# Performance work log

Measured on AMD Instinct MI355X. Metric: run time of the kernel, lower is better.

The kernel has to match this reference:

```python
import jax, jax.numpy as jnp
import numpy as np


def setup_inputs() -> dict:
    key = jax.random.key(0)
    k1, k2 = jax.random.split(key)
    N = 2_000_000
    rotation = jax.random.normal(k1, (N, 3, 3), dtype=jnp.float32)
    # learned parameter: eye(3) + 0.001 * randn(3,3)
    mat = jnp.eye(3, dtype=jnp.float32) + 0.001 * jax.random.normal(k2, (3, 3), dtype=jnp.float32)
    return {"rotation": rotation, "mat": mat}


def reference(rotation, mat):
    # new_mat[n] = rotation[n] @ mat   (mat broadcast over the batch)
    new_mat = jnp.einsum('nab,bc->nac', rotation, mat)
    # batched 3x3 SVD; polar orthogonal factor U @ V^T
    U, S, Vh = jnp.linalg.svd(new_mat, full_matrices=False)
    out = jnp.einsum('nab,nbc->nac', U, Vh)  # Vh is already V^T
    logdet = jnp.zeros((rotation.shape[0],), dtype=rotation.dtype)
    return out, logdet
```

## Files before the change

### kernel.cpp

```cpp
#include <hip/hip_runtime.h>
#include <math.h>

constexpr int BLOCK = 256;

__global__ __launch_bounds__(BLOCK) void polar3x3_kernel(
    const float* __restrict__ rot,
    const float* __restrict__ mat,
    float* __restrict__ outq,
    float* __restrict__ logdet,
    int N)
{
    __shared__ float lds[BLOCK * 9];
    const int tid = threadIdx.x;
    const long long base = (long long)blockIdx.x * BLOCK;
    const int rem = (int)(N - base);
    const int nmat = rem < BLOCK ? rem : BLOCK;
    const int nflt = nmat * 9;
    const int nv4 = nflt >> 2;

    const float* gsrc = rot + base * 9;
    {
        const float4* g4 = (const float4*)gsrc;
        float4* l4 = (float4*)lds;
        for (int i = tid; i < nv4; i += BLOCK) l4[i] = g4[i];
        for (int i = (nv4 << 2) + tid; i < nflt; i += BLOCK) lds[i] = gsrc[i];
    }

    const float m0=mat[0], m1=mat[1], m2=mat[2], m3=mat[3], m4=mat[4],
                m5=mat[5], m6=mat[6], m7=mat[7], m8=mat[8];
    const double dM = (double)m0*((double)m4*m8-(double)m5*m7)
                    - (double)m1*((double)m3*m8-(double)m5*m6)
                    + (double)m2*((double)m3*m7-(double)m4*m6);
    __syncthreads();

    const bool active = tid < nmat;
    float x0=1.f,x1=0.f,x2=0.f,x3=0.f,x4=1.f,x5=0.f,x6=0.f,x7=0.f,x8=1.f;
    float detA = 1.f;

    if (active) {
        const float* r = &lds[tid * 9];
        const float r0=r[0],r1=r[1],r2=r[2],r3=r[3],r4=r[4],r5=r[5],r6=r[6],r7=r[7],r8=r[8];
        const double dR = (double)r0*((double)r4*r8-(double)r5*r7)
                        - (double)r1*((double)r3*r8-(double)r5*r6)
                        + (double)r2*((double)r3*r7-(double)r4*r6);
        detA = (float)(dR * dM);
        x0=fmaf(r0,m0,fmaf(r1,m3,r2*m6));
        x1=fmaf(r0,m1,fmaf(r1,m4,r2*m7));
        x2=fmaf(r0,m2,fmaf(r1,m5,r2*m8));
        x3=fmaf(r3,m0,fmaf(r4,m3,r5*m6));
        x4=fmaf(r3,m1,fmaf(r4,m4,r5*m7));
        x5=fmaf(r3,m2,fmaf(r4,m5,r5*m8));
        x6=fmaf(r6,m0,fmaf(r7,m3,r8*m6));
        x7=fmaf(r6,m1,fmaf(r7,m4,r8*m7));
        x8=fmaf(r6,m2,fmaf(r7,m5,r8*m8));
    }

    #pragma unroll
    for (int it = 0; it < 5; ++it) {
        const float c0=fmaf(x4,x8,-x5*x7), c1=fmaf(x5,x6,-x3*x8), c2=fmaf(x3,x7,-x4*x6);
        const float c3=fmaf(x2,x7,-x1*x8), c4=fmaf(x0,x8,-x2*x6), c5=fmaf(x1,x6,-x0*x7);
        const float c6=fmaf(x1,x5,-x2*x4), c7=fmaf(x2,x3,-x0*x5), c8=fmaf(x0,x4,-x1*x3);
        const float det = (it==0) ? detA : fmaf(x0,c0,fmaf(x1,c1,x2*c2));
        const float adet = fmaxf(fabsf(det), 1e-30f);
        float nX2, nC2;
        { const float a=fmaf(x1,x1,x0*x0), b=fmaf(x3,x3,x2*x2),
                      e=fmaf(x5,x5,x4*x4), d=fmaf(x7,x7,x6*x6);
          nX2=(a+b)+(e+fmaf(x8,x8,d)); }
        { const float a=fmaf(c1,c1,c0*c0), b=fmaf(c3,c3,c2*c2),
                      e=fmaf(c5,c5,c4*c4), d=fmaf(c7,c7,c6*c6);
          nC2=(a+b)+(e+fmaf(c8,c8,d)); }
        const float h  = __builtin_amdgcn_rsqf(adet);
        const float pr = __builtin_amdgcn_sqrtf(__builtin_amdgcn_sqrtf(
                             nC2*__builtin_amdgcn_rcpf(nX2)));
        const float qr = __builtin_amdgcn_sqrtf(__builtin_amdgcn_sqrtf(
                             nX2*__builtin_amdgcn_rcpf(nC2)));
        const float s = 0.5f*pr*h;
        const float t = copysignf(0.5f*qr*h, det);
        x0=fmaf(s,x0,t*c0); x1=fmaf(s,x1,t*c1); x2=fmaf(s,x2,t*c2);
        x3=fmaf(s,x3,t*c3); x4=fmaf(s,x4,t*c4); x5=fmaf(s,x5,t*c5);
        x6=fmaf(s,x6,t*c6); x7=fmaf(s,x7,t*c7); x8=fmaf(s,x8,t*c8);
    }
    {
        const float c0=fmaf(x4,x8,-x5*x7), c1=fmaf(x5,x6,-x3*x8), c2=fmaf(x3,x7,-x4*x6);
        const float c3=fmaf(x2,x7,-x1*x8), c4=fmaf(x0,x8,-x2*x6), c5=fmaf(x1,x6,-x0*x7);
        const float c6=fmaf(x1,x5,-x2*x4), c7=fmaf(x2,x3,-x0*x5), c8=fmaf(x0,x4,-x1*x3);
        const float det = fmaf(x0,c0,fmaf(x1,c1,x2*c2));
        const float t = 0.5f*__builtin_amdgcn_rcpf(det);
        x0=fmaf(0.5f,x0,t*c0); x1=fmaf(0.5f,x1,t*c1); x2=fmaf(0.5f,x2,t*c2);
        x3=fmaf(0.5f,x3,t*c3); x4=fmaf(0.5f,x4,t*c4); x5=fmaf(0.5f,x5,t*c5);
        x6=fmaf(0.5f,x6,t*c6); x7=fmaf(0.5f,x7,t*c7); x8=fmaf(0.5f,x8,t*c8);
    }

    if (active) {
        float* w = &lds[tid * 9];
        w[0]=x0; w[1]=x1; w[2]=x2; w[3]=x3; w[4]=x4;
        w[5]=x5; w[6]=x6; w[7]=x7; w[8]=x8;
    }
    __syncthreads();

    float* gdst = outq + base * 9;
    {
        float4* g4 = (float4*)gdst;
        const float4* l4 = (const float4*)lds;
        for (int i = tid; i < nv4; i += BLOCK) g4[i] = l4[i];
        for (int i = (nv4 << 2) + tid; i < nflt; i += BLOCK) gdst[i] = lds[i];
    }

    if (base + tid < N) logdet[base + tid] = 0.0f;
}

extern "C" void kernel_launch(void* const* d_in, const int* in_sizes, int n_in,
                              void* d_out, int out_size, void* d_ws, size_t ws_size,
                              hipStream_t stream) {
    const float* rot = (const float*)d_in[0];
    const float* mat = (const float*)d_in[1];
    float* out = (float*)d_out;
    const int N = in_sizes[0] / 9;
    float* logdet = out + (long long)N * 9;
    const int nblocks = (N + BLOCK - 1) / BLOCK;
    polar3x3_kernel<<<nblocks, BLOCK, 0, stream>>>(rot, mat, out, logdet, N);
}
```

Measured before the change: 138.1 us.

## Use per-wave direct global-to-LDS loads and drop block barriers

Each wave now stages its own 64 matrices through a private LDS slice, loading them with global_load_lds (direct DMA into LDS, no VGPR round trip) and waiting with s_waitcnt instead of __syncthreads. Block-wide barriers are gone, so waves proceed independently. A separate path handles the partial tail wave with direct per-thread global loads and stores. The cost is reliance on exact LDS layout and manual waitcnt correctness, plus an added code path for the tail.

```diff
diff --git a/kernel.cpp b/kernel.cpp
--- a/kernel.cpp
+++ b/kernel.cpp
@@ -3,57 +3,35 @@
 
 constexpr int BLOCK = 256;
 
-__global__ __launch_bounds__(BLOCK) void polar3x3_kernel(
-    const float* __restrict__ rot,
-    const float* __restrict__ mat,
-    float* __restrict__ outq,
-    float* __restrict__ logdet,
-    int N)
+typedef __attribute__((address_space(3))) uint32_t lds_u32_t;
+typedef __attribute__((address_space(1))) const uint32_t glb_u32_t;
+
+__device__ __forceinline__ void polar_core(
+    const float r0, const float r1, const float r2,
+    const float r3, const float r4, const float r5,
+    const float r6, const float r7, const float r8,
+    const float m0, const float m1, const float m2,
+    const float m3, const float m4, const float m5,
+    const float m6, const float m7, const float m8,
+    const double dM,
+    float& x0, float& x1, float& x2,
+    float& x3, float& x4, float& x5,
+    float& x6, float& x7, float& x8)
 {
-    __shared__ float lds[BLOCK * 9];
-    const int tid = threadIdx.x;
-    const long long base = (long long)blockIdx.x * BLOCK;
-    const int rem = (int)(N - base);
-    const int nmat = rem < BLOCK ? rem : BLOCK;
-    const int nflt = nmat * 9;
-    const int nv4 = nflt >> 2;
+    const double dR = (double)r0*((double)r4*r8-(double)r5*r7)
+                    - (double)r1*((double)r3*r8-(double)r5*r6)
+                    + (double)r2*((double)r3*r7-(double)r4*r6);
+    const float detA = (float)(dR * dM);
 
-    const float* gsrc = rot + base * 9;
-    {
-        const float4* g4 = (const float4*)gsrc;
-        float4* l4 = (float4*)lds;
-        for (int i = tid; i < nv4; i += BLOCK) l4[i] = g4[i];
-        for (int i = (nv4 << 2) + tid; i < nflt; i += BLOCK) lds[i] = gsrc[i];
-    }
-
-    const float m0=mat[0], m1=mat[1], m2=mat[2], m3=mat[3], m4=mat[4],
-                m5=mat[5], m6=mat[6], m7=mat[7], m8=mat[8];
-    const double dM = (double)m0*((double)m4*m8-(double)m5*m7)
-                    - (double)m1*((double)m3*m8-(double)m5*m6)
-                    + (double)m2*((double)m3*m7-(double)m4*m6);
-    __syncthreads();
-
-    const bool active = tid < nmat;
-    float x0=1.f,x1=0.f,x2=0.f,x3=0.f,x4=1.f,x5=0.f,x6=0.f,x7=0.f,x8=1.f;
-    float detA = 1.f;
-
-    if (active) {
-        const float* r = &lds[tid * 9];
-        const float r0=r[0],r1=r[1],r2=r[2],r3=r[3],r4=r[4],r5=r[5],r6=r[6],r7=r[7],r8=r[8];
-        const double dR = (double)r0*((double)r4*r8-(double)r5*r7)
-                        - (double)r1*((double)r3*r8-(double)r5*r6)
-                        + (double)r2*((double)r3*r7-(double)r4*r6);
-        detA = (float)(dR * dM);
-        x0=fmaf(r0,m0,fmaf(r1,m3,r2*m6));
-        x1=fmaf(r0,m1,fmaf(r1,m4,r2*m7));
-        x2=fmaf(r0,m2,fmaf(r1,m5,r2*m8));
-        x3=fmaf(r3,m0,fmaf(r4,m3,r5*m6));
-        x4=fmaf(r3,m1,fmaf(r4,m4,r5*m7));
-        x5=fmaf(r3,m2,fmaf(r4,m5,r5*m8));
-        x6=fmaf(r6,m0,fmaf(r7,m3,r8*m6));
-        x7=fmaf(r6,m1,fmaf(r7,m4,r8*m7));
-        x8=fmaf(r6,m2,fmaf(r7,m5,r8*m8));
-    }
+    x0=fmaf(r0,m0,fmaf(r1,m3,r2*m6));
+    x1=fmaf(r0,m1,fmaf(r1,m4,r2*m7));
+    x2=fmaf(r0,m2,fmaf(r1,m5,r2*m8));
+    x3=fmaf(r3,m0,fmaf(r4,m3,r5*m6));
+    x4=fmaf(r3,m1,fmaf(r4,m4,r5*m7));
+    x5=fmaf(r3,m2,fmaf(r4,m5,r5*m8));
+    x6=fmaf(r6,m0,fmaf(r7,m3,r8*m6));
+    x7=fmaf(r6,m1,fmaf(r7,m4,r8*m7));
+    x8=fmaf(r6,m2,fmaf(r7,m5,r8*m8));
 
     #pragma unroll
     for (int it = 0; it < 5; ++it) {
@@ -90,23 +68,81 @@
         x3=fmaf(0.5f,x3,t*c3); x4=fmaf(0.5f,x4,t*c4); x5=fmaf(0.5f,x5,t*c5);
         x6=fmaf(0.5f,x6,t*c6); x7=fmaf(0.5f,x7,t*c7); x8=fmaf(0.5f,x8,t*c8);
     }
+}
 
-    if (active) {
-        float* w = &lds[tid * 9];
+__global__ __launch_bounds__(BLOCK) void polar3x3_kernel(
+    const float* __restrict__ rot,
+    const float* __restrict__ mat,
+    float* __restrict__ outq,
+    float* __restrict__ logdet,
+    int N)
+{
+    __shared__ float lds[BLOCK * 9];
+    const int tid  = threadIdx.x;
+    const int lane = tid & 63;
+    const int wave = tid >> 6;
+    const long long wbase = (long long)blockIdx.x * BLOCK + (long long)wave * 64;
+    if (wbase >= N) return;
+
+    float* wlds = lds + wave * 576;
+
+    const float m0=mat[0], m1=mat[1], m2=mat[2], m3=mat[3], m4=mat[4],
+                m5=mat[5], m6=mat[6], m7=mat[7], m8=mat[8];
+    const double dM = (double)m0*((double)m4*m8-(double)m5*m7)
+                    - (double)m1*((double)m3*m8-(double)m5*m6)
+                    + (double)m2*((double)m3*m7-(double)m4*m6);
+
+    const long long nrem = N - wbase;
+    if (nrem >= 64) {
+        {
+            const char* g = (const char*)(rot + wbase * 9);
+            __builtin_amdgcn_global_load_lds((glb_u32_t*)(g + (size_t)lane * 16),
+                                             (lds_u32_t*)wlds, 16, 0, 0);
+            __builtin_amdgcn_global_load_lds((glb_u32_t*)(g + 1024 + (size_t)lane * 16),
+                                             (lds_u32_t*)(wlds + 256), 16, 0, 0);
+            __builtin_amdgcn_global_load_lds((glb_u32_t*)(g + 2048 + (size_t)lane * 4),
+                                             (lds_u32_t*)(wlds + 512), 4, 0, 0);
+        }
+        asm volatile("s_waitcnt vmcnt(0)" ::: "memory");
+
+        const float* r = &wlds[lane * 9];
+        const float r0=r[0],r1=r[1],r2=r[2],r3=r[3],r4=r[4],
+                    r5=r[5],r6=r[6],r7=r[7],r8=r[8];
+
+        float x0,x1,x2,x3,x4,x5,x6,x7,x8;
+        polar_core(r0,r1,r2,r3,r4,r5,r6,r7,r8,
+                   m0,m1,m2,m3,m4,m5,m6,m7,m8, dM,
+                   x0,x1,x2,x3,x4,x5,x6,x7,x8);
+
+        float* w = &wlds[lane * 9];
         w[0]=x0; w[1]=x1; w[2]=x2; w[3]=x3; w[4]=x4;
         w[5]=x5; w[6]=x6; w[7]=x7; w[8]=x8;
+        asm volatile("s_waitcnt lgkmcnt(0)" ::: "memory");
+
+        float* gdst = outq + wbase * 9;
+        const float4* l4 = (const float4*)wlds;
+        float4* g4 = (float4*)gdst;
+        g4[lane]        = l4[lane];
+        g4[64 + lane]   = l4[64 + lane];
+        gdst[512 + lane] = wlds[512 + lane];
+        logdet[wbase + lane] = 0.0f;
+    } else {
+        const bool act = lane < (int)nrem;
+        float r0=1.f,r1=0.f,r2=0.f,r3=0.f,r4=1.f,r5=0.f,r6=0.f,r7=0.f,r8=1.f;
+        const float* gsrc = rot + (wbase + lane) * 9;
+        if (act) { r0=gsrc[0];r1=gsrc[1];r2=gsrc[2];r3=gsrc[3];r4=gsrc[4];
+                   r5=gsrc[5];r6=gsrc[6];r7=gsrc[7];r8=gsrc[8]; }
+        float x0,x1,x2,x3,x4,x5,x6,x7,x8;
+        polar_core(r0,r1,r2,r3,r4,r5,r6,r7,r8,
+                   m0,m1,m2,m3,m4,m5,m6,m7,m8, dM,
+                   x0,x1,x2,x3,x4,x5,x6,x7,x8);
+        if (act) {
+            float* gdst = outq + (wbase + lane) * 9;
+            gdst[0]=x0; gdst[1]=x1; gdst[2]=x2; gdst[3]=x3; gdst[4]=x4;
+            gdst[5]=x5; gdst[6]=x6; gdst[7]=x7; gdst[8]=x8;
+            logdet[wbase + lane] = 0.0f;
+        }
     }
-    __syncthreads();
-
-    float* gdst = outq + base * 9;
-    {
-        float4* g4 = (float4*)gdst;
-        const float4* l4 = (const float4*)lds;
-        for (int i = tid; i < nv4; i += BLOCK) g4[i] = l4[i];
-        for (int i = (nv4 << 2) + tid; i < nflt; i += BLOCK) gdst[i] = lds[i];
-    }
-
-    if (base + tid < N) logdet[base + tid] = 0.0f;
 }
 
 extern "C" void kernel_launch(void* const* d_in, const int* in_sizes, int n_in,
```

Measured after the change: 142.0 us. 2.8% more time.
